# Kernel tuning notes

Measured on AMD Instinct MI355X. Metric: run time of the kernel, lower is better.

## Reference

```python
import jax, jax.numpy as jnp
import numpy as np

N, H, VOCAB = 512, 512, 32000

def setup_inputs() -> dict:
    key = jax.random.key(0)
    ks = jax.random.split(key, 7)
    s1 = 1.0 / np.sqrt(N)
    s2 = 1.0 / np.sqrt(H)
    return {
        "r_l": jax.random.normal(ks[0], (4, 256, N), dtype=jnp.float32),
        "W1": jax.random.uniform(ks[1], (H, N), jnp.float32, -s1, s1),
        "b1": jax.random.uniform(ks[2], (H,), jnp.float32, -s1, s1),
        "W2": jax.random.uniform(ks[3], (H * N, H), jnp.float32, -s2, s2),
        "b2": jax.random.uniform(ks[4], (H * N,), jnp.float32, -s2, s2),
        "W_out": jax.random.uniform(ks[5], (VOCAB, H), jnp.float32, -s2, s2),
        "b_out": jax.random.uniform(ks[6], (VOCAB,), jnp.float32, -s2, s2),
    }

def reference(r_l, W1, b1, W2, b2, W_out, b_out):
    B, L, n = r_l.shape
    r = r_l.reshape(B * L, n)                      # (T, N)
    x = jax.nn.relu(r @ W1.T + b1)                 # (T, H)
    W_att = (x @ W2.T + b2).reshape(-1, H, N)      # (T, H, N) per-token weights
    r_ol = jnp.einsum('thn,tn->th', W_att, r)      # batched GEMV
    logits = r_ol @ W_out.T + b_out                # (T, vocab)
    return logits.reshape(B, L, VOCAB)
```

## Files before the change

### kernel.cpp

```cpp
#include <hip/hip_runtime.h>
#include <hip/hip_bf16.h>

typedef __attribute__((ext_vector_type(8))) short short8;
typedef __attribute__((ext_vector_type(4))) short short4v;
typedef __attribute__((ext_vector_type(4))) float floatx4;

static __device__ __forceinline__ unsigned short f2bf(float f){
  union { float f; unsigned int u; } v; v.f = f;
  return (unsigned short)((v.u + 0x7FFFu + ((v.u >> 16) & 1u)) >> 16);
}
static __device__ __forceinline__ float bf2f(unsigned short b){
  union { unsigned int u; float f; } v; v.u = ((unsigned int)b) << 16; return v.f;
}
static __device__ __forceinline__ short8 cvt8_pk(floatx4 a, floatx4 b){
  union { __hip_bfloat162 h[4]; short8 s; } u;
  u.h[0] = __float22bfloat162_rn(float2{a[0], a[1]});
  u.h[1] = __float22bfloat162_rn(float2{a[2], a[3]});
  u.h[2] = __float22bfloat162_rn(float2{b[0], b[1]});
  u.h[3] = __float22bfloat162_rn(float2{b[2], b[3]});
  return u.s;
}
static __device__ __forceinline__ short4v cvt4(floatx4 a){
  union { __hip_bfloat162 h[2]; short4v s; } u;
  u.h[0] = __float22bfloat162_rn(float2{a[0], a[1]});
  u.h[1] = __float22bfloat162_rn(float2{a[2], a[3]});
  return u.s;
}
static __device__ __forceinline__ short8 frag_ld(const char* ldsbase, int row, int kbyte){
  return *(const short8*)(ldsbase + row*256 + (kbyte ^ ((row & 15) << 4)));
}
static __device__ __forceinline__ short8 frag_ld64(const char* base, int row, int kbyte){
  return *(const short8*)(base + row*128 + (kbyte ^ ((row & 7) << 4)));
}

template<int ROWS>
static __device__ __forceinline__ void stage_tile(char* ldsbase, const float* __restrict__ src,
                                                  int ld, int tid){
  #pragma unroll
  for (int w = 0; w < ROWS/32; ++w){
    int g = w*512 + tid;
    int row = g >> 4, k8 = g & 15;
    const float* p = src + (size_t)row*ld + k8*8;
    floatx4 v0 = *(const floatx4*)p;
    floatx4 v1 = *(const floatx4*)(p+4);
    *(short8*)(ldsbase + row*256 + ((k8*16) ^ ((row & 15) << 4))) = cvt8_pk(v0, v1);
  }
}

template<int MODE>
__global__ __launch_bounds__(512)
void gemm_plain(const float* __restrict__ Asrc, const float* __restrict__ Bsrc,
                const float* __restrict__ bias, void* __restrict__ out, int out_ld){
  __shared__ char smem[98304];
  char* At = smem;
  char* Bt = smem + 65536;
  const int tid  = threadIdx.x;
  const int lane = tid & 63, w = tid >> 6;
  const int wm = w & 3, wn = w >> 2;
  const int bid = blockIdx.x;
  const int t0 = (bid & 3) * 256;
  const int c0 = (bid >> 2) * 128;
  const int rbase = wm*64, cbase = wn*64;

  floatx4 acc[4][4];
  #pragma unroll
  for (int i=0;i<4;++i)
    #pragma unroll
    for (int j=0;j<4;++j) acc[i][j] = floatx4{0.f,0.f,0.f,0.f};

  for (int kb = 0; kb < 4; ++kb){
    __syncthreads();
    stage_tile<256>(At, Asrc + (size_t)t0*512 + kb*128, 512, tid);
    stage_tile<128>(Bt, Bsrc + (size_t)c0*512 + kb*128, 512, tid);
    __syncthreads();
    #pragma unroll
    for (int ks = 0; ks < 4; ++ks){
      const int kbyte = (ks*32 + (lane>>4)*8) * 2;
      short8 af[4], bfr[4];
      #pragma unroll
      for (int mi=0; mi<4; ++mi) af[mi] = frag_ld(At, rbase + mi*16 + (lane&15), kbyte);
      #pragma unroll
      for (int ni=0; ni<4; ++ni) bfr[ni] = frag_ld(Bt, cbase + ni*16 + (lane&15), kbyte);
      #pragma unroll
      for (int mi=0; mi<4; ++mi)
        #pragma unroll
        for (int ni=0; ni<4; ++ni)
          acc[mi][ni] = __builtin_amdgcn_mfma_f32_16x16x32_bf16(af[mi], bfr[ni], acc[mi][ni], 0,0,0);
    }
  }
  #pragma unroll
  for (int mi=0; mi<4; ++mi){
    #pragma unroll
    for (int ni=0; ni<4; ++ni){
      #pragma unroll
      for (int rg=0; rg<4; ++rg){
        int t = t0 + rbase + mi*16 + (lane>>4)*4 + rg;
        int c = c0 + cbase + ni*16 + (lane&15);
        float v = acc[mi][ni][rg];
        if (MODE == 0){
          v += bias[c]; v = v > 0.f ? v : 0.f;
          ((unsigned short*)out)[(size_t)t*out_ld + c] = f2bf(v);
        } else {
          ((float*)out)[(size_t)t*out_ld + c] = v;
        }
      }
    }
  }
}

__global__ __launch_bounds__(512)
void k2_fold(const unsigned short* __restrict__ xbf, const float* __restrict__ r,
             const float* __restrict__ W2, float* __restrict__ r_ol){
  __shared__ char smem[147456];
  unsigned short* RT2 = (unsigned short*)(smem + 131072);
  const int tid  = threadIdx.x;
  const int lane = tid & 63, w = tid >> 6;
  const int wm = w & 3, wn = w >> 2;
  const int bid = blockIdx.x;
  const int xr = bid & 7, idx = bid >> 3;
  const int m  = idx & 3, gh = idx >> 2;
  const int g  = xr + 8*gh;
  const int ht = g & 3, ns = g >> 2;
  const int t0 = m*256, h0 = ht*128, n0 = ns*32;

  #pragma unroll
  for (int i = 0; i < 16; ++i){
    int e = i*512 + tid; int row = e >> 5, c = e & 31;
    RT2[c*256 + row] = f2bf(r[(size_t)(t0+row)*512 + n0 + c]);
  }

  floatx4 acc[4][4];
  #pragma unroll
  for (int i=0;i<4;++i)
    #pragma unroll
    for (int j=0;j<4;++j) acc[i][j] = floatx4{0.f,0.f,0.f,0.f};

  floatx4 lb[8];

  auto stageA = [&](int kb2){
    const int chunk = tid & 15, rbase_ = tid >> 4;
    #pragma unroll
    for (int j = 0; j < 8; ++j){
      const int row = rbase_ + j*32;
      short8 v = *(const short8*)(xbf + (size_t)(t0+row)*512 + kb2*128 + chunk*8);
      *(short8*)(smem + row*256 + (((chunk ^ (row & 15)) << 4))) = v;
    }
  };
  auto issueB = [&](int n, int kb2){
    const int c16 = tid & 31, rb = tid >> 5;
    const float* base = W2 + (size_t)(n0+n)*512 + (size_t)kb2*128 + c16*4;
    #pragma unroll
    for (int j = 0; j < 8; ++j)
      lb[j] = *(const floatx4*)(base + (size_t)(h0 + rb + j*16)*262144);
  };
  auto cvtB = [&](char* Bb){
    const int c8 = tid & 31, rb = tid >> 5;
    #pragma unroll
    for (int j = 0; j < 8; ++j){
      const int row = rb + j*16;
      const int byte = (((c8 >> 1) ^ (row & 15)) << 4) | ((c8 & 1) << 3);
      *(short4v*)(Bb + row*256 + byte) = cvt4(lb[j]);
    }
  };
  auto compute_fold = [&](const char* Bb, int n){
    float rvv[4][4];
    #pragma unroll
    for (int mi = 0; mi < 4; ++mi){
      const int rrow = wm*64 + mi*16 + (lane>>4)*4;
      short4v tv = *(const short4v*)(RT2 + n*256 + rrow);
      #pragma unroll
      for (int j = 0; j < 4; ++j) rvv[mi][j] = bf2f((unsigned short)tv[j]);
    }
    floatx4 ct[4][4];
    #pragma unroll
    for (int ks = 0; ks < 4; ++ks){
      const int kbyte = ks*64 + (lane>>4)*16;
      short8 af[4], bfr[4];
      #pragma unroll
      for (int mi=0; mi<4; ++mi) af[mi] = frag_ld(smem, wm*64 + mi*16 + (lane&15), kbyte);
      #pragma unroll
      for (int ni=0; ni<4; ++ni) bfr[ni] = frag_ld(Bb, wn*64 + ni*16 + (lane&15), kbyte);
      __builtin_amdgcn_s_setprio(1);
      #pragma unroll
      for (int mi=0; mi<4; ++mi)
        #pragma unroll
        for (int ni=0; ni<4; ++ni)
          ct[mi][ni] = __builtin_amdgcn_mfma_f32_16x16x32_bf16(
              af[mi], bfr[ni], (ks==0) ? floatx4{0.f,0.f,0.f,0.f} : ct[mi][ni], 0,0,0);
      __builtin_amdgcn_s_setprio(0);
    }
    #pragma unroll
    for (int mi=0; mi<4; ++mi)
      #pragma unroll
      for (int ni=0; ni<4; ++ni){
        acc[mi][ni][0] += rvv[mi][0] * ct[mi][ni][0];
        acc[mi][ni][1] += rvv[mi][1] * ct[mi][ni][1];
        acc[mi][ni][2] += rvv[mi][2] * ct[mi][ni][2];
        acc[mi][ni][3] += rvv[mi][3] * ct[mi][ni][3];
      }
  };

  stageA(0);
  issueB(0, 0);
  cvtB(smem + 65536);
  __syncthreads();

  int cur = 0;
  for (int kb2 = 0; kb2 < 4; ++kb2){
    for (int n = 0; n < 32; ++n){
      const int bi = kb2*32 + n;
      if (bi < 127){
        const int nn = (n == 31) ? 0 : n + 1;
        const int nk = (n == 31) ? kb2 + 1 : kb2;
        issueB(nn, nk);
      }
      compute_fold(smem + 65536 + cur*32768, n);
      if (bi < 127) cvtB(smem + 65536 + (cur^1)*32768);
      __syncthreads();
      cur ^= 1;
    }
    if (kb2 < 3){
      stageA(kb2 + 1);
      __syncthreads();
    }
  }

  #pragma unroll
  for (int ni = 0; ni < 4; ++ni){
    const int h = h0 + wn*64 + ni*16 + (lane & 15);
    #pragma unroll
    for (int mi = 0; mi < 4; ++mi){
      #pragma unroll
      for (int rg = 0; rg < 4; ++rg){
        const int t = t0 + wm*64 + mi*16 + (lane >> 4)*4 + rg;
        atomicAdd(&r_ol[(size_t)t*512 + h], acc[mi][ni][rg]);
      }
    }
  }
}

__global__ __launch_bounds__(512, 2)
void gemm_out(const float* __restrict__ Asrc, const float* __restrict__ Bsrc,
              const float* __restrict__ bias, float* __restrict__ out){
  __shared__ char smem[98304];
  const int tid  = threadIdx.x;
  const int lane = tid & 63, w = tid >> 6;
  const int wm = w & 3, wn = w >> 2;
  const int bid = blockIdx.x;
  const int t0 = (bid & 3) * 256;
  const int c0 = (bid >> 2) * 128;

  floatx4 acc[4][4];
  #pragma unroll
  for (int i=0;i<4;++i)
    #pragma unroll
    for (int j=0;j<4;++j) acc[i][j] = floatx4{0.f,0.f,0.f,0.f};

  floatx4 la[8], lb[4];
  const int r16 = tid >> 4, c4 = tid & 15;

  auto issue = [&](int s){
    const int K0 = s*64;
    #pragma unroll
    for (int it=0; it<8; ++it){
      int row = it*32 + r16;
      la[it] = *(const floatx4*)(Asrc + (size_t)(t0+row)*512 + K0 + c4*4);
    }
    #pragma unroll
    for (int it=0; it<4; ++it){
      int row = it*32 + r16;
      lb[it] = *(const floatx4*)(Bsrc + (size_t)(c0+row)*512 + K0 + c4*4);
    }
  };
  auto write_buf = [&](int buf){
    char* ad = smem + buf*32768;
    #pragma unroll
    for (int it=0; it<8; ++it){
      int row = it*32 + r16;
      *(short4v*)(ad + row*128 + ((c4*8) ^ ((row & 7) << 4))) = cvt4(la[it]);
    }
    char* bd = smem + 65536 + buf*16384;
    #pragma unroll
    for (int it=0; it<4; ++it){
      int row = it*32 + r16;
      *(short4v*)(bd + row*128 + ((c4*8) ^ ((row & 7) << 4))) = cvt4(lb[it]);
    }
  };
  auto compute = [&](int buf){
    const char* Ab = smem + buf*32768;
    const char* Bb = smem + 65536 + buf*16384;
    #pragma unroll
    for (int ks = 0; ks < 2; ++ks){
      const int kbyte = ks*64 + (lane >> 4)*16;
      short8 af[4], bfr[4];
      #pragma unroll
      for (int mi = 0; mi < 4; ++mi) af[mi] = frag_ld64(Ab, wm*64 + mi*16 + (lane&15), kbyte);
      #pragma unroll
      for (int ni = 0; ni < 4; ++ni) bfr[ni] = frag_ld64(Bb, wn*64 + ni*16 + (lane&15), kbyte);
      __builtin_amdgcn_s_setprio(1);
      #pragma unroll
      for (int mi = 0; mi < 4; ++mi)
        #pragma unroll
        for (int ni = 0; ni < 4; ++ni)
          acc[mi][ni] = __builtin_amdgcn_mfma_f32_16x16x32_bf16(af[mi], bfr[ni], acc[mi][ni], 0,0,0);
      __builtin_amdgcn_s_setprio(0);
    }
  };

  issue(0);
  write_buf(0);
  __syncthreads();
  for (int s = 0; s < 8; ++s){
    const int cur = s & 1;
    if (s < 7) issue(s + 1);
    compute(cur);
    if (s < 7){
      write_buf(cur ^ 1);
      __syncthreads();
    }
  }

  #pragma unroll
  for (int ni = 0; ni < 4; ++ni){
    const int c = c0 + wn*64 + ni*16 + (lane & 15);
    const float bv = bias[c];
    #pragma unroll
    for (int mi = 0; mi < 4; ++mi){
      #pragma unroll
      for (int rg = 0; rg < 4; ++rg){
        const int t = t0 + wm*64 + mi*16 + (lane >> 4)*4 + rg;
        out[(size_t)t*32000 + c] = acc[mi][ni][rg] + bv;
      }
    }
  }
}

extern "C" void kernel_launch(void* const* d_in, const int* in_sizes, int n_in,
                              void* d_out, int out_size, void* d_ws, size_t ws_size,
                              hipStream_t stream) {
  const float* r    = (const float*)d_in[0];
  const float* W1   = (const float*)d_in[1];
  const float* b1   = (const float*)d_in[2];
  const float* W2   = (const float*)d_in[3];
  const float* b2   = (const float*)d_in[4];
  const float* Wout = (const float*)d_in[5];
  const float* bout = (const float*)d_in[6];
  float* logits = (float*)d_out;

  unsigned short* x_bf = (unsigned short*)d_ws;
  float* r_ol = (float*)((char*)d_ws + 1024*512*2);

  gemm_plain<0><<<16, 512, 0, stream>>>(r, W1, b1, x_bf, 512);
  gemm_plain<1><<<16, 512, 0, stream>>>(r, b2, nullptr, r_ol, 512);
  k2_fold<<<256, 512, 0, stream>>>(x_bf, r, W2, r_ol);
  gemm_out<<<1000, 512, 0, stream>>>(r_ol, Wout, bout, logits);
}
```

Before: 405.7 us.

## Halve k2_fold tile depth and n-slice to fit two blocks per CU

Shrinks the fold kernel's per-block tile: each block now handles 16 n-columns instead of 32, and the K chunk drops from 128 to 64. The grid doubles to 512 blocks. LDS use drops from 144 KB to 72 KB, so two blocks can be resident per CU, which should hide the latency of streaming the large W2 tensor. The staging, swizzle and B-load layouts are rewritten for 128-byte rows with packed 8-element conversion. In exchange it doubles the atomicAdd traffic into r_ol and adds more loop iterations and barriers per block.

```diff
diff --git a/kernel.cpp b/kernel.cpp
--- a/kernel.cpp
+++ b/kernel.cpp
@@ -111,8 +111,8 @@
 __global__ __launch_bounds__(512)
 void k2_fold(const unsigned short* __restrict__ xbf, const float* __restrict__ r,
              const float* __restrict__ W2, float* __restrict__ r_ol){
-  __shared__ char smem[147456];
-  unsigned short* RT2 = (unsigned short*)(smem + 131072);
+  __shared__ char smem[73728];
+  unsigned short* RT2 = (unsigned short*)(smem + 65536);
   const int tid  = threadIdx.x;
   const int lane = tid & 63, w = tid >> 6;
   const int wm = w & 3, wn = w >> 2;
@@ -121,11 +121,11 @@
   const int m  = idx & 3, gh = idx >> 2;
   const int g  = xr + 8*gh;
   const int ht = g & 3, ns = g >> 2;
-  const int t0 = m*256, h0 = ht*128, n0 = ns*32;
-
-  #pragma unroll
-  for (int i = 0; i < 16; ++i){
-    int e = i*512 + tid; int row = e >> 5, c = e & 31;
+  const int t0 = m*256, h0 = ht*128, n0 = ns*16;
+
+  #pragma unroll
+  for (int i = 0; i < 8; ++i){
+    int e = i*512 + tid; int row = e >> 4, c = e & 15;
     RT2[c*256 + row] = f2bf(r[(size_t)(t0+row)*512 + n0 + c]);
   }
 
@@ -135,31 +135,30 @@
     #pragma unroll
     for (int j=0;j<4;++j) acc[i][j] = floatx4{0.f,0.f,0.f,0.f};
 
-  floatx4 lb[8];
-
-  auto stageA = [&](int kb2){
-    const int chunk = tid & 15, rbase_ = tid >> 4;
-    #pragma unroll
-    for (int j = 0; j < 8; ++j){
-      const int row = rbase_ + j*32;
-      short8 v = *(const short8*)(xbf + (size_t)(t0+row)*512 + kb2*128 + chunk*8);
-      *(short8*)(smem + row*256 + (((chunk ^ (row & 15)) << 4))) = v;
-    }
-  };
-  auto issueB = [&](int n, int kb2){
-    const int c16 = tid & 31, rb = tid >> 5;
-    const float* base = W2 + (size_t)(n0+n)*512 + (size_t)kb2*128 + c16*4;
-    #pragma unroll
-    for (int j = 0; j < 8; ++j)
-      lb[j] = *(const floatx4*)(base + (size_t)(h0 + rb + j*16)*262144);
+  floatx4 lb[4];
+  const int seg = tid & 7, rb = tid >> 3;
+
+  auto stageA = [&](int kb){
+    #pragma unroll
+    for (int j = 0; j < 4; ++j){
+      const int row = rb + j*64;
+      short8 v = *(const short8*)(xbf + (size_t)(t0+row)*512 + kb*64 + seg*8);
+      *(short8*)(smem + row*128 + ((seg*16) ^ ((row & 7) << 4))) = v;
+    }
+  };
+  auto issueB = [&](int n, int kb){
+    #pragma unroll
+    for (int j = 0; j < 2; ++j){
+      const float* p = W2 + (size_t)(h0 + rb + j*64)*262144 + (size_t)(n0+n)*512 + kb*64 + seg*8;
+      lb[j*2]   = *(const floatx4*)p;
+      lb[j*2+1] = *(const floatx4*)(p+4);
+    }
   };
   auto cvtB = [&](char* Bb){
-    const int c8 = tid & 31, rb = tid >> 5;
-    #pragma unroll
-    for (int j = 0; j < 8; ++j){
-      const int row = rb + j*16;
-      const int byte = (((c8 >> 1) ^ (row & 15)) << 4) | ((c8 & 1) << 3);
-      *(short4v*)(Bb + row*256 + byte) = cvt4(lb[j]);
+    #pragma unroll
+    for (int j = 0; j < 2; ++j){
+      const int row = rb + j*64;
+      *(short8*)(Bb + row*128 + ((seg*16) ^ ((row & 7) << 4))) = cvt8_pk(lb[j*2], lb[j*2+1]);
     }
   };
   auto compute_fold = [&](const char* Bb, int n){
@@ -173,13 +172,13 @@
     }
     floatx4 ct[4][4];
     #pragma unroll
-    for (int ks = 0; ks < 4; ++ks){
+    for (int ks = 0; ks < 2; ++ks){
       const int kbyte = ks*64 + (lane>>4)*16;
       short8 af[4], bfr[4];
       #pragma unroll
-      for (int mi=0; mi<4; ++mi) af[mi] = frag_ld(smem, wm*64 + mi*16 + (lane&15), kbyte);
-      #pragma unroll
-      for (int ni=0; ni<4; ++ni) bfr[ni] = frag_ld(Bb, wn*64 + ni*16 + (lane&15), kbyte);
+      for (int mi=0; mi<4; ++mi) af[mi] = frag_ld64(smem, wm*64 + mi*16 + (lane&15), kbyte);
+      #pragma unroll
+      for (int ni=0; ni<4; ++ni) bfr[ni] = frag_ld64(Bb, wn*64 + ni*16 + (lane&15), kbyte);
       __builtin_amdgcn_s_setprio(1);
       #pragma unroll
       for (int mi=0; mi<4; ++mi)
@@ -202,25 +201,25 @@
 
   stageA(0);
   issueB(0, 0);
-  cvtB(smem + 65536);
+  cvtB(smem + 32768);
   __syncthreads();
 
   int cur = 0;
-  for (int kb2 = 0; kb2 < 4; ++kb2){
-    for (int n = 0; n < 32; ++n){
-      const int bi = kb2*32 + n;
+  for (int kb = 0; kb < 8; ++kb){
+    for (int n = 0; n < 16; ++n){
+      const int bi = kb*16 + n;
       if (bi < 127){
-        const int nn = (n == 31) ? 0 : n + 1;
-        const int nk = (n == 31) ? kb2 + 1 : kb2;
+        const int nn = (n == 15) ? 0 : n + 1;
+        const int nk = (n == 15) ? kb + 1 : kb;
         issueB(nn, nk);
       }
-      compute_fold(smem + 65536 + cur*32768, n);
-      if (bi < 127) cvtB(smem + 65536 + (cur^1)*32768);
+      compute_fold(smem + 32768 + cur*16384, n);
+      if (bi < 127) cvtB(smem + 32768 + (cur^1)*16384);
       __syncthreads();
       cur ^= 1;
     }
-    if (kb2 < 3){
-      stageA(kb2 + 1);
+    if (kb < 7){
+      stageA(kb + 1);
       __syncthreads();
     }
   }
@@ -352,6 +351,6 @@
 
   gemm_plain<0><<<16, 512, 0, stream>>>(r, W1, b1, x_bf, 512);
   gemm_plain<1><<<16, 512, 0, stream>>>(r, b2, nullptr, r_ol, 512);
-  k2_fold<<<256, 512, 0, stream>>>(x_bf, r, W2, r_ol);
+  k2_fold<<<512, 512, 0, stream>>>(x_bf, r, W2, r_ol);
   gemm_out<<<1000, 512, 0, stream>>>(r_ol, Wout, bout, logits);
 }
```

New measurement: 444.2 us. 9.5% more time.
